# Performance work log

Hardware: AMD Instinct MI355X
Metric: run time of the kernel (lower is better)

## Reference

```python
import jax, jax.numpy as jnp
import numpy as np

N, T, S, E, H, DFF = 4, 2048, 2048, 512, 8, 2048
DH = E // H
EPS = 1e-5


def layer_norm(x, w, b):
    m = jnp.mean(x, axis=-1, keepdims=True)
    v = jnp.mean(jnp.square(x - m), axis=-1, keepdims=True)
    return (x - m) * jax.lax.rsqrt(v + EPS) * w + b


def mha(q, k, v, wq, bq, wk, bk, wv, bv, wo, bo, mask=None):
    # q: (N,Tq,E), k/v: (N,Tk,E); torch Linear convention: y = x @ W.T + b
    Nq, Tq, _ = q.shape
    Tk = k.shape[1]
    Q = (q @ wq.T + bq).reshape(Nq, Tq, H, DH).transpose(0, 2, 1, 3)  # (N,H,Tq,DH)
    K = (k @ wk.T + bk).reshape(Nq, Tk, H, DH).transpose(0, 2, 1, 3)
    V = (v @ wv.T + bv).reshape(Nq, Tk, H, DH).transpose(0, 2, 1, 3)
    scores = jnp.einsum('bhtd,bhsd->bhts', Q, K) * (1.0 / np.sqrt(DH))  # (N,H,Tq,Tk)
    if mask is not None:
        scores = jnp.where(mask, scores, jnp.float32(-1e9))
    attn = jax.nn.softmax(scores, axis=-1)
    out = jnp.einsum('bhts,bhsd->bhtd', attn, V)  # (N,H,Tq,DH)
    out = out.transpose(0, 2, 1, 3).reshape(Nq, Tq, E)
    return out @ wo.T + bo


def setup_inputs() -> dict:
    key = jax.random.key(0)
    ks = jax.random.split(key, 20)
    s = 0.02

    def lin(k, out_d, in_d):
        return jax.random.normal(k, (out_d, in_d), jnp.float32) * s

    inp = {
        'tgt': jax.random.normal(ks[0], (N, T, E), jnp.float32),
        'memory': jax.random.normal(ks[1], (N, S, E), jnp.float32),
        'tgt_mask': jnp.tril(jnp.ones((T, T), dtype=bool)),  # causal (T,T)
        # self-attention params
        'sa_wq': lin(ks[2], E, E), 'sa_bq': jnp.zeros((E,), jnp.float32),
        'sa_wk': lin(ks[3], E, E), 'sa_bk': jnp.zeros((E,), jnp.float32),
        'sa_wv': lin(ks[4], E, E), 'sa_bv': jnp.zeros((E,), jnp.float32),
        'sa_wo': lin(ks[5], E, E), 'sa_bo': jnp.zeros((E,), jnp.float32),
        # cross-attention params
        'ca_wq': lin(ks[6], E, E), 'ca_bq': jnp.zeros((E,), jnp.float32),
        'ca_wk': lin(ks[7], E, E), 'ca_bk': jnp.zeros((E,), jnp.float32),
        'ca_wv': lin(ks[8], E, E), 'ca_bv': jnp.zeros((E,), jnp.float32),
        'ca_wo': lin(ks[9], E, E), 'ca_bo': jnp.zeros((E,), jnp.float32),
        # FFN params
        'w1': lin(ks[10], DFF, E), 'b1': jnp.zeros((DFF,), jnp.float32),
        'w2': lin(ks[11], E, DFF), 'b2': jnp.zeros((E,), jnp.float32),
        # LayerNorm params
        'ln1_w': jnp.ones((E,), jnp.float32), 'ln1_b': jnp.zeros((E,), jnp.float32),
        'ln2_w': jnp.ones((E,), jnp.float32), 'ln2_b': jnp.zeros((E,), jnp.float32),
        'ln3_w': jnp.ones((E,), jnp.float32), 'ln3_b': jnp.zeros((E,), jnp.float32),
    }
    return inp


def reference(tgt, memory, tgt_mask,
              sa_wq, sa_bq, sa_wk, sa_bk, sa_wv, sa_bv, sa_wo, sa_bo,
              ca_wq, ca_bq, ca_wk, ca_bk, ca_wv, ca_bv, ca_wo, ca_bo,
              w1, b1, w2, b2,
              ln1_w, ln1_b, ln2_w, ln2_b, ln3_w, ln3_b):
    # stage 1: masked self-attention + residual + LN (dropout=0 / eval mode)
    sa = mha(tgt, tgt, tgt, sa_wq, sa_bq, sa_wk, sa_bk, sa_wv, sa_bv, sa_wo, sa_bo, mask=tgt_mask)
    x = layer_norm(tgt + sa, ln1_w, ln1_b)
    # stage 2: cross-attention over encoder memory + residual + LN
    ca = mha(x, memory, memory, ca_wq, ca_bq, ca_wk, ca_bk, ca_wv, ca_bv, ca_wo, ca_bo)
    x = layer_norm(x + ca, ln2_w, ln2_b)
    # stage 3: FFN (ReLU) + residual + LN
    mlp = jax.nn.relu(x @ w1.T + b1) @ w2.T + b2
    out = layer_norm(x + mlp, ln3_w, ln3_b)
    return out
```

## Files before the change

kernel.cpp:

```cpp
#include <hip/hip_runtime.h>
#include <hip/hip_bf16.h>
#include <cstdint>

typedef short short8 __attribute__((ext_vector_type(8)));
typedef short short4v __attribute__((ext_vector_type(4)));
typedef float f32x4 __attribute__((ext_vector_type(4)));
typedef float f32x16 __attribute__((ext_vector_type(16)));

#define GLL16(gp, lp) __builtin_amdgcn_global_load_lds( \
    (const __attribute__((address_space(1))) unsigned int*)(gp), \
    (__attribute__((address_space(3))) unsigned int*)(lp), 16, 0, 0)
#define WAITV(n) asm volatile("s_waitcnt vmcnt(" #n ")" ::: "memory")

__device__ __forceinline__ float bf2f(ushort u) {
    union { unsigned int i; float f; } v; v.i = ((unsigned int)u) << 16; return v.f;
}
__device__ __forceinline__ ushort f2bf(float f) {
    union { float f; unsigned int u; } v; v.f = f;
    unsigned int r = v.u + 0x7FFFu + ((v.u >> 16) & 1u);
    return (ushort)(r >> 16);
}
__device__ __forceinline__ int cvtpk_bf16(float lo, float hi) {
    int r;
    asm("v_cvt_pk_bf16_f32 %0, %1, %2" : "=v"(r) : "v"(lo), "v"(hi));
    return r;
}
__device__ __forceinline__ void plane32_swap(int& a, int& b) {
    asm volatile("v_permlane32_swap_b32 %0, %1" : "+v"(a), "+v"(b));
}
__device__ __forceinline__ float fast_exp2(float x) {
    float r;
    asm("v_exp_f32 %0, %1" : "=v"(r) : "v"(x));
    return r;
}

#define SCQ 0.18033688f

struct CvtArgs {
    const float* src[12];
    ushort*      dst[12];
};
__global__ __launch_bounds__(256) void f2b_all(CvtArgs a)
{
    int id = blockIdx.x;
    int seg, boff;
    if (id < 4096)       { seg = 0; boff = id; }
    else if (id < 8192)  { seg = 1; boff = id - 4096; }
    else if (id < 10240) { int t = id - 8192; seg = 2 + (t >> 8); boff = t & 255; }
    else if (id < 11264) { seg = 10; boff = id - 10240; }
    else                 { seg = 11; boff = id - 11264; }
    int i = (boff * 256 + threadIdx.x) * 4;
    f32x4 v = *(const f32x4*)(a.src[seg] + i);
    short4v o;
#pragma unroll
    for (int e = 0; e < 4; ++e) o[e] = (short)f2bf(v[e]);
    *(short4v*)(a.dst[seg] + i) = o;
}

template<int MODE, int DEPTH, int TN>
__global__ __launch_bounds__(256) void gemm_bt(
    const ushort* __restrict__ A, const ushort* __restrict__ W,
    const float* __restrict__ b0, const float* __restrict__ b1,
    const float* __restrict__ b2,
    ushort* __restrict__ C0, ushort* __restrict__ C1, ushort* __restrict__ C2,
    int M, int N, int K)
{
    constexpr int NI = TN / 32;
    constexpr int L  = (TN == 128) ? 4 : 3;
    __shared__ ushort As[DEPTH][128 * 32];
    __shared__ ushort Bs[DEPTH][TN * 32];
    const int tid = threadIdx.x;
    const int l  = tid & 63;
    const int w  = tid >> 6;
    const int wr = w >> 1, wc = w & 1;
    const int bn = blockIdx.x, bm = blockIdx.y;
    const int lg = l >> 4, li = l & 15;

    const ushort* Ab = A + (size_t)(bm * 128) * K;
    const ushort* Bb = W + (size_t)(bn * TN) * K;

    f32x4 acc[4][NI] = {};

    const int r0 = tid >> 2,         s0 = (tid & 3) ^ ((r0 >> 2) & 3);
    const int r1 = (tid + 256) >> 2, s1 = (tid & 3) ^ ((r1 >> 2) & 3);

    auto stage = [&](int buf, int kt) {
        const ushort* Ak = Ab + kt * 32;
        const ushort* Bk = Bb + kt * 32;
        GLL16(Ak + (size_t)r0 * K + s0 * 8, &As[buf][tid * 8]);
        GLL16(Ak + (size_t)r1 * K + s1 * 8, &As[buf][(tid + 256) * 8]);
        GLL16(Bk + (size_t)r0 * K + s0 * 8, &Bs[buf][tid * 8]);
        if (TN == 128)
            GLL16(Bk + (size_t)r1 * K + s1 * 8, &Bs[buf][(tid + 256) * 8]);
    };

    const int nk = K >> 5;
#pragma unroll
    for (int p = 0; p < DEPTH - 1; ++p)
        if (p < nk) stage(p, p);

    for (int kt = 0; kt < nk; ++kt) {
        const int b = kt & (DEPTH - 1);
        const int nxt = kt + DEPTH - 1;
        if (nxt < nk) stage(nxt & (DEPTH - 1), nxt);
        const int rem = nk - 1 - kt;
        const int fl = rem < DEPTH - 1 ? rem : DEPTH - 1;
        if (L == 4) {
            if (fl >= 3)      WAITV(12);
            else if (fl == 2) WAITV(8);
            else if (fl == 1) WAITV(4);
            else              WAITV(0);
        } else {
            if (fl >= 3)      WAITV(9);
            else if (fl == 2) WAITV(6);
            else if (fl == 1) WAITV(3);
            else              WAITV(0);
        }
        __builtin_amdgcn_s_barrier();
        __builtin_amdgcn_sched_barrier(0);

        short8 af[4], bfr[NI];
#pragma unroll
        for (int mi = 0; mi < 4; ++mi) {
            int row = wr * 64 + mi * 16 + li;
            int ch  = lg ^ ((row >> 2) & 3);
            af[mi] = *(const short8*)(&As[b][row * 32 + ch * 8]);
        }
#pragma unroll
        for (int ni = 0; ni < NI; ++ni) {
            int row = wc * (TN / 2) + ni * 16 + li;
            int ch  = lg ^ ((row >> 2) & 3);
            bfr[ni] = *(const short8*)(&Bs[b][row * 32 + ch * 8]);
        }
#pragma unroll
        for (int mi = 0; mi < 4; ++mi)
#pragma unroll
            for (int ni = 0; ni < NI; ++ni)
                acc[mi][ni] = __builtin_amdgcn_mfma_f32_16x16x32_bf16(
                    af[mi], bfr[ni], acc[mi][ni], 0, 0, 0);

        __builtin_amdgcn_sched_barrier(0);
        asm volatile("s_waitcnt lgkmcnt(0)" ::: "memory");
        __builtin_amdgcn_s_barrier();
    }

    const int crow0 = bm * 128 + wr * 64 + lg * 4;
    const int ccol0 = bn * TN + wc * (TN / 2) + li;
    const int sec = (MODE == 2 || MODE == 3) ? (bn >> 2) : 0;
    const float* bp = b0;
    ushort* Cw = C0;
    bool vsec = false;
    if (MODE == 2) {
        bp = (sec == 0) ? b0 : (sec == 1) ? b1 : b2;
        Cw = (sec == 0) ? C0 : (sec == 1) ? C1 : C2;
        vsec = (sec == 2);
    } else if (MODE == 3) {
        bp = (sec == 0) ? b0 : b1;
        Cw = (sec == 0) ? C0 : C1;
        vsec = (sec == 1);
    }
    const int Nout = (MODE == 2 || MODE == 3) ? 512 : N;
    const float scl = (MODE == 4 || (MODE == 2 && sec == 0)) ? SCQ : 1.f;

#pragma unroll
    for (int ni = 0; ni < NI; ++ni) {
        int col = ccol0 + ni * 16;
        int cl  = (MODE == 2 || MODE == 3) ? (col & 511) : col;
        float bv = bp[cl];
#pragma unroll
        for (int mi = 0; mi < 4; ++mi) {
            int row = crow0 + mi * 16;
            if (vsec) {
                int n = row >> 11, t = row & 2047;
                int h = cl >> 6,  d = cl & 63;
                size_t base = ((size_t)((n * 8 + h) * 64 + d)) * 2048 + t;
                short4v pk;
#pragma unroll
                for (int r = 0; r < 4; ++r) pk[r] = (short)f2bf(acc[mi][ni][r] + bv);
                *(short4v*)(Cw + base) = pk;
            } else {
#pragma unroll
                for (int r = 0; r < 4; ++r) {
                    float v = (acc[mi][ni][r] + bv) * scl;
                    if (MODE == 1) v = fmaxf(v, 0.f);
                    Cw[(size_t)(row + r) * Nout + cl] = f2bf(v);
                }
            }
        }
    }
}

template<bool CAUSAL>
__global__ __launch_bounds__(256) void attn_kernel(
    const ushort* __restrict__ Q, const ushort* __restrict__ K,
    const ushort* __restrict__ Vt, ushort* __restrict__ P0,
    ushort* __restrict__ P1, float* __restrict__ Ls, int Tk)
{
    __shared__ ushort SH[24576];
    const int tid = threadIdx.x;
    const int l = tid & 63, wq = tid >> 6;
    const int c = l & 31, hi = l >> 5;

    int qt, nh, ck;
    if (CAUSAL) {
        int g = (int)blockIdx.x >> 6;
        qt = (g < 8) ? (15 - g) : (g - 8);
        int r = blockIdx.x & 63;
        nh = r >> 1; ck = r & 1;
    } else {
        int pos = ((int)blockIdx.x & 7) * 128 + ((int)blockIdx.x >> 3);
        nh = pos >> 5; ck = (pos >> 4) & 1; qt = pos & 15;
    }
    const int q0 = qt * 128;
    const int n = nh >> 3, h = nh & 7;
    const int qw = q0 + wq * 32;
    const int qrow = qw + c;

    short8 qf[4];
#pragma unroll
    for (int s = 0; s < 4; ++s)
        qf[s] = *(const short8*)(Q + (size_t)(n * 2048 + qrow) * 512
                                   + h * 64 + s * 16 + hi * 8);

    f32x16 oacc[2] = {};
    f32x16 oS = {};
    const short ONE = (short)0x3F80;
    const short8 ones = {ONE, ONE, ONE, ONE, ONE, ONE, ONE, ONE};

    const ushort* Kbase = K + (size_t)(n * 2048) * 512 + h * 64;
    const ushort* Vbase = Vt + (size_t)nh * 64 * Tk;

    const int rowA = tid >> 3;
    const int cs0 = (((tid & 7) - (rowA >> 3)) & 7) ^ (rowA & 7);
    const int cs1 = (((tid & 7) - (rowA >> 3) + 4) & 7) ^ (rowA & 7);

    auto stage = [&](int buf, int j0) {
        ushort* kd = SH + buf * 4096;
        ushort* vd = SH + 12288 + buf * 4096;
        GLL16(Kbase + (size_t)(j0 + rowA) * 512 + cs0 * 8,      kd + tid * 8);
        GLL16(Kbase + (size_t)(j0 + rowA + 32) * 512 + cs1 * 8, kd + (tid + 256) * 8);
        GLL16(Vbase + (size_t)rowA * Tk + j0 + cs0 * 8,         vd + tid * 8);
        GLL16(Vbase + (size_t)(rowA + 32) * Tk + j0 + cs1 * 8,  vd + (tid + 256) * 8);
    };

    const int total = CAUSAL ? (2 * qt + 2) : (Tk >> 6);
    const int start = (ck * total) >> 1;
    const int cnt   = (((ck + 1) * total) >> 1) - start;

    if (cnt > 0) stage(0, start << 6);
    if (cnt > 1) stage(1, (start + 1) << 6);

    for (int s = 0; s < cnt; ++s) {
        const int b  = s % 3;
        const int j0 = (start + s) << 6;
        if (s + 1 < cnt) {
            WAITV(4);
        } else {
            WAITV(0);
        }
        __builtin_amdgcn_s_barrier();
        __builtin_amdgcn_sched_barrier(0);
        if (s + 2 < cnt) stage((s + 2) % 3, (start + s + 2) << 6);

        const bool active = !CAUSAL || (j0 < qw + 32);
        if (active) {
            const ushort* kls = SH + b * 4096;
            const ushort* vls = SH + 12288 + b * 4096;
            const bool domask = CAUSAL && (j0 + 64 > qw);

            f32x16 sacc[2] = {};
            __builtin_amdgcn_s_setprio(1);
#pragma unroll
            for (int ks = 0; ks < 4; ++ks) {
#pragma unroll
                for (int t2 = 0; t2 < 2; ++t2) {
                    int row = t2 * 32 + c;
                    int ch  = (((ks * 2 + hi) ^ (row & 7)) + (row >> 3)) & 7;
                    short8 kf = *(const short8*)(kls + row * 64 + ch * 8);
                    sacc[t2] = __builtin_amdgcn_mfma_f32_32x32x16_bf16(
                        kf, qf[ks], sacc[t2], 0, 0, 0);
                }
            }
            __builtin_amdgcn_s_setprio(0);

#pragma unroll
            for (int t2 = 0; t2 < 2; ++t2) {
                float pv[16];
#pragma unroll
                for (int reg = 0; reg < 16; ++reg) {
                    float p = fast_exp2(sacc[t2][reg]);
                    if (domask) {
                        int jg = j0 + t2 * 32 + (reg & 3) + 8 * (reg >> 2) + 4 * hi;
                        if (jg > qrow) p = 0.f;
                    }
                    pv[reg] = p;
                }
                int X0 = cvtpk_bf16(pv[0],  pv[1]),  Y0 = cvtpk_bf16(pv[2],  pv[3]);
                int X1 = cvtpk_bf16(pv[4],  pv[5]),  Y1 = cvtpk_bf16(pv[6],  pv[7]);
                int X2 = cvtpk_bf16(pv[8],  pv[9]),  Y2 = cvtpk_bf16(pv[10], pv[11]);
                int X3 = cvtpk_bf16(pv[12], pv[13]), Y3 = cvtpk_bf16(pv[14], pv[15]);
                plane32_swap(X0, X1); plane32_swap(Y0, Y1);
                plane32_swap(X2, X3); plane32_swap(Y2, Y3);
                union { int i[4]; short8 s; } pa0 = {{X0, Y0, X1, Y1}},
                                              pa1 = {{X2, Y2, X3, Y3}};
                __builtin_amdgcn_s_setprio(1);
                oS = __builtin_amdgcn_mfma_f32_32x32x16_bf16(pa0.s, ones, oS, 0, 0, 0);
                oS = __builtin_amdgcn_mfma_f32_32x32x16_bf16(pa1.s, ones, oS, 0, 0, 0);
#pragma unroll
                for (int sp = 0; sp < 2; ++sp) {
                    short8 pa = sp ? pa1.s : pa0.s;
#pragma unroll
                    for (int dc = 0; dc < 2; ++dc) {
                        int row = dc * 32 + c;
                        int ch  = (((t2 * 4 + sp * 2 + hi) ^ (row & 7)) + (row >> 3)) & 7;
                        short8 vb = *(const short8*)(vls + row * 64 + ch * 8);
                        oacc[dc] = __builtin_amdgcn_mfma_f32_32x32x16_bf16(
                            pa, vb, oacc[dc], 0, 0, 0);
                    }
                }
                __builtin_amdgcn_s_setprio(0);
            }
        }

        __builtin_amdgcn_sched_barrier(0);
        asm volatile("s_waitcnt lgkmcnt(0)" ::: "memory");
    }
    WAITV(0);

    ushort* Pw = ck ? P1 : P0;
    if (c == 0) {
#pragma unroll
        for (int reg = 0; reg < 16; ++reg) {
            int qloc = (reg & 3) + 8 * (reg >> 2) + 4 * hi;
            Ls[ck * 65536 + nh * 2048 + qw + qloc] = oS[reg];
        }
    }
#pragma unroll
    for (int dc = 0; dc < 2; ++dc)
#pragma unroll
        for (int reg = 0; reg < 16; ++reg) {
            int qloc = (reg & 3) + 8 * (reg >> 2) + 4 * hi;
            size_t off = (size_t)(n * 2048 + qw + qloc) * 512
                       + h * 64 + dc * 32 + c;
            Pw[off] = f2bf(oacc[dc][reg]);
        }
}

__global__ __launch_bounds__(256) void attn_merge(
    const ushort* __restrict__ P0, const ushort* __restrict__ P1,
    const float* __restrict__ Ls, ushort* __restrict__ out)
{
    const int row = blockIdx.x * 4 + (threadIdx.x >> 6);
    const int l = threadIdx.x & 63;
    const size_t off = (size_t)row * 512 + l * 8;
    const int n = row >> 11, q = row & 2047, h = l >> 3;
    const int lidx = (n * 8 + h) * 2048 + q;
    float linv = 1.f / (Ls[lidx] + Ls[65536 + lidx]);
    short8 a = *(const short8*)(P0 + off);
    short8 b = *(const short8*)(P1 + off);
    short8 o;
#pragma unroll
    for (int e = 0; e < 8; ++e)
        o[e] = (short)f2bf((bf2f((ushort)a[e]) + bf2f((ushort)b[e])) * linv);
    *(short8*)(out + off) = o;
}

template<int F32OUT>
__global__ __launch_bounds__(256) void ln_kernel(
    const ushort* __restrict__ X, const ushort* __restrict__ Y,
    const float* __restrict__ W, const float* __restrict__ B,
    void* __restrict__ outp)
{
    const int row = blockIdx.x * 4 + (threadIdx.x >> 6);
    const int l = threadIdx.x & 63;
    const size_t off = (size_t)row * 512 + l * 8;
    short8 xv = *(const short8*)(X + off);
    short8 yv = *(const short8*)(Y + off);
    float v[8], s = 0.f, s2 = 0.f;
#pragma unroll
    for (int e = 0; e < 8; ++e) {
        float f = bf2f((ushort)xv[e]) + bf2f((ushort)yv[e]);
        v[e] = f; s += f; s2 += f * f;
    }
#pragma unroll
    for (int m = 1; m < 64; m <<= 1) {
        s  += __shfl_xor(s,  m);
        s2 += __shfl_xor(s2, m);
    }
    float mean = s * (1.f / 512.f);
    float var  = s2 * (1.f / 512.f) - mean * mean;
    float rs   = rsqrtf(var + 1e-5f);
    f32x4 w0 = *(const f32x4*)(W + l * 8);
    f32x4 w1 = *(const f32x4*)(W + l * 8 + 4);
    f32x4 b0 = *(const f32x4*)(B + l * 8);
    f32x4 b1 = *(const f32x4*)(B + l * 8 + 4);
    float wv[8] = {w0[0], w0[1], w0[2], w0[3], w1[0], w1[1], w1[2], w1[3]};
    float bv[8] = {b0[0], b0[1], b0[2], b0[3], b1[0], b1[1], b1[2], b1[3]};
    if (F32OUT) {
        float* out = (float*)outp;
#pragma unroll
        for (int e = 0; e < 8; ++e)
            out[off + e] = (v[e] - mean) * rs * wv[e] + bv[e];
    } else {
        ushort* out = (ushort*)outp;
        short8 ov;
#pragma unroll
        for (int e = 0; e < 8; ++e)
            ov[e] = (short)f2bf((v[e] - mean) * rs * wv[e] + bv[e]);
        *(short8*)(out + off) = ov;
    }
}

extern "C" void kernel_launch(void* const* d_in, const int* in_sizes, int n_in,
                              void* d_out, int out_size, void* d_ws, size_t ws_size,
                              hipStream_t stream)
{
    (void)in_sizes; (void)n_in; (void)out_size; (void)ws_size;
    const float* tgt  = (const float*)d_in[0];
    const float* mem  = (const float*)d_in[1];
    const float* sa_wq = (const float*)d_in[3];
    const float* sa_bq = (const float*)d_in[4];
    const float* sa_wk = (const float*)d_in[5];
    const float* sa_bk = (const float*)d_in[6];
    const float* sa_wv = (const float*)d_in[7];
    const float* sa_bv = (const float*)d_in[8];
    const float* sa_wo = (const float*)d_in[9];
    const float* sa_bo = (const float*)d_in[10];
    const float* ca_wq = (const float*)d_in[11];
    const float* ca_bq = (const float*)d_in[12];
    const float* ca_wk = (const float*)d_in[13];
    const float* ca_bk = (const float*)d_in[14];
    const float* ca_wv = (const float*)d_in[15];
    const float* ca_bv = (const float*)d_in[16];
    const float* ca_wo = (const float*)d_in[17];
    const float* ca_bo = (const float*)d_in[18];
    const float* w1    = (const float*)d_in[19];
    const float* b1    = (const float*)d_in[20];
    const float* w2    = (const float*)d_in[21];
    const float* b2    = (const float*)d_in[22];
    const float* ln1w  = (const float*)d_in[23];
    const float* ln1b  = (const float*)d_in[24];
    const float* ln2w  = (const float*)d_in[25];
    const float* ln2b  = (const float*)d_in[26];
    const float* ln3w  = (const float*)d_in[27];
    const float* ln3b  = (const float*)d_in[28];

    const size_t SE = (size_t)8192 * 512;
    const size_t EE = (size_t)512 * 512;
    ushort* ws = (ushort*)d_ws;
    ushort* Wb   = ws;
    ushort* bsqkv = Wb;
    ushort* bswo  = Wb + 3 * EE;
    ushort* bcwq  = Wb + 4 * EE;
    ushort* bckv  = Wb + 5 * EE;
    ushort* bcwo  = Wb + 7 * EE;
    ushort* bw1   = Wb + 8 * EE;
    ushort* bw2   = bw1 + 4 * EE;
    ushort* tgtb = Wb + 16 * EE;
    ushort* memb = tgtb + SE;
    ushort* Qb   = memb + SE;
    ushort* Kb   = Qb + SE;
    ushort* Vb   = Kb + SE;
    ushort* X1   = Vb + SE;
    ushort* AO   = X1 + SE;
    float*  LsBuf = (float*)(AO + SE);
    ushort* PO   = Qb;
    ushort* X2   = tgtb;
    ushort* Hb   = Qb;

    dim3 blk(256);
    dim3 gqkv(12, 64);
    dim3 gkv(8, 64);
    dim3 g64n(8, 64);
    dim3 g2048(16, 64);
    dim3 ga(1024);
    dim3 gln(2048);

    CvtArgs ca;
    ca.src[0] = tgt;    ca.dst[0] = tgtb;
    ca.src[1] = mem;    ca.dst[1] = memb;
    ca.src[2] = sa_wq;  ca.dst[2] = bsqkv;
    ca.src[3] = sa_wk;  ca.dst[3] = bsqkv + EE;
    ca.src[4] = sa_wv;  ca.dst[4] = bsqkv + 2 * EE;
    ca.src[5] = sa_wo;  ca.dst[5] = bswo;
    ca.src[6] = ca_wq;  ca.dst[6] = bcwq;
    ca.src[7] = ca_wk;  ca.dst[7] = bckv;
    ca.src[8] = ca_wv;  ca.dst[8] = bckv + EE;
    ca.src[9] = ca_wo;  ca.dst[9] = bcwo;
    ca.src[10] = w1;    ca.dst[10] = bw1;
    ca.src[11] = w2;    ca.dst[11] = bw2;
    f2b_all<<<12288, blk, 0, stream>>>(ca);

    gemm_bt<2, 2, 128><<<gqkv, blk, 0, stream>>>(tgtb, bsqkv, sa_bq, sa_bk, sa_bv,
                                                 Qb, Kb, Vb, 8192, 1536, 512);
    attn_kernel<true><<<ga, blk, 0, stream>>>(Qb, Kb, Vb, AO, X1, LsBuf, 2048);
    attn_merge<<<gln, blk, 0, stream>>>(AO, X1, LsBuf, AO);
    gemm_bt<0, 4, 64><<<g64n, blk, 0, stream>>>(AO, bswo, sa_bo, nullptr, nullptr,
                                                PO, nullptr, nullptr, 8192, 512, 512);
    ln_kernel<0><<<gln, blk, 0, stream>>>(tgtb, PO, ln1w, ln1b, X1);

    gemm_bt<4, 4, 64><<<g64n, blk, 0, stream>>>(X1, bcwq, ca_bq, nullptr, nullptr,
                                                Qb, nullptr, nullptr, 8192, 512, 512);
    gemm_bt<3, 2, 128><<<gkv, blk, 0, stream>>>(memb, bckv, ca_bk, ca_bv, nullptr,
                                                Kb, Vb, nullptr, 8192, 1024, 512);
    attn_kernel<false><<<ga, blk, 0, stream>>>(Qb, Kb, Vb, AO, tgtb, LsBuf, 2048);
    attn_merge<<<gln, blk, 0, stream>>>(AO, tgtb, LsBuf, AO);
    gemm_bt<0, 4, 64><<<g64n, blk, 0, stream>>>(AO, bcwo, ca_bo, nullptr, nullptr,
                                                PO, nullptr, nullptr, 8192, 512, 512);
    ln_kernel<0><<<gln, blk, 0, stream>>>(X1, PO, ln2w, ln2b, X2);

    gemm_bt<1, 2, 128><<<g2048, blk, 0, stream>>>(X2, bw1, b1, nullptr, nullptr,
                                                  Hb, nullptr, nullptr, 8192, 2048, 512);
    gemm_bt<0, 4, 64><<<g64n, blk, 0, stream>>>(Hb, bw2, b2, nullptr, nullptr,
                                                AO, nullptr, nullptr, 8192, 512, 2048);
    ln_kernel<1><<<gln, blk, 0, stream>>>(X2, AO, ln3w, ln3b, d_out);
}
```

Before: 295.6 us.

## Split-K the N=512 output GEMMs and sum partials inside LayerNorm

```diff
diff --git a/kernel.cpp b/kernel.cpp
--- a/kernel.cpp
+++ b/kernel.cpp
@@ -74,10 +74,12 @@
     const int w  = tid >> 6;
     const int wr = w >> 1, wc = w & 1;
     const int bn = blockIdx.x, bm = blockIdx.y;
+    const int kz = (MODE == 5) ? blockIdx.z : 0;
+    const int Keff = (MODE == 5) ? (K >> 1) : K;
     const int lg = l >> 4, li = l & 15;
 
-    const ushort* Ab = A + (size_t)(bm * 128) * K;
-    const ushort* Bb = W + (size_t)(bn * TN) * K;
+    const ushort* Ab = A + (size_t)(bm * 128) * K + (size_t)kz * Keff;
+    const ushort* Bb = W + (size_t)(bn * TN) * K + (size_t)kz * Keff;
 
     f32x4 acc[4][NI] = {};
 
@@ -94,7 +96,7 @@
             GLL16(Bk + (size_t)r1 * K + s1 * 8, &Bs[buf][(tid + 256) * 8]);
     };
 
-    const int nk = K >> 5;
+    const int nk = Keff >> 5;
 #pragma unroll
     for (int p = 0; p < DEPTH - 1; ++p)
         if (p < nk) stage(p, p);
@@ -158,6 +160,8 @@
         bp = (sec == 0) ? b0 : b1;
         Cw = (sec == 0) ? C0 : C1;
         vsec = (sec == 1);
+    } else if (MODE == 5) {
+        Cw = kz ? C1 : C0;
     }
     const int Nout = (MODE == 2 || MODE == 3) ? 512 : N;
     const float scl = (MODE == 4 || (MODE == 2 && sec == 0)) ? SCQ : 1.f;
@@ -166,7 +170,7 @@
     for (int ni = 0; ni < NI; ++ni) {
         int col = ccol0 + ni * 16;
         int cl  = (MODE == 2 || MODE == 3) ? (col & 511) : col;
-        float bv = bp[cl];
+        float bv = (MODE == 5 && kz) ? 0.f : bp[cl];
 #pragma unroll
         for (int mi = 0; mi < 4; ++mi) {
             int row = crow0 + mi * 16;
@@ -365,9 +369,10 @@
     *(short8*)(out + off) = o;
 }
 
-template<int F32OUT>
+template<int F32OUT, int NY>
 __global__ __launch_bounds__(256) void ln_kernel(
     const ushort* __restrict__ X, const ushort* __restrict__ Y,
+    const ushort* __restrict__ Y2,
     const float* __restrict__ W, const float* __restrict__ B,
     void* __restrict__ outp)
 {
@@ -376,10 +381,13 @@
     const size_t off = (size_t)row * 512 + l * 8;
     short8 xv = *(const short8*)(X + off);
     short8 yv = *(const short8*)(Y + off);
+    short8 y2v = {};
+    if (NY == 2) y2v = *(const short8*)(Y2 + off);
     float v[8], s = 0.f, s2 = 0.f;
 #pragma unroll
     for (int e = 0; e < 8; ++e) {
         float f = bf2f((ushort)xv[e]) + bf2f((ushort)yv[e]);
+        if (NY == 2) f += bf2f((ushort)y2v[e]);
         v[e] = f; s += f; s2 += f * f;
     }
 #pragma unroll
@@ -464,7 +472,6 @@
     ushort* X1   = Vb + SE;
     ushort* AO   = X1 + SE;
     float*  LsBuf = (float*)(AO + SE);
-    ushort* PO   = Qb;
     ushort* X2   = tgtb;
     ushort* Hb   = Qb;
 
@@ -472,6 +479,7 @@
     dim3 gqkv(12, 64);
     dim3 gkv(8, 64);
     dim3 g64n(8, 64);
+    dim3 g64k2(8, 64, 2);
     dim3 g2048(16, 64);
     dim3 ga(1024);
     dim3 gln(2048);
@@ -495,9 +503,9 @@
                                                  Qb, Kb, Vb, 8192, 1536, 512);
     attn_kernel<true><<<ga, blk, 0, stream>>>(Qb, Kb, Vb, AO, X1, LsBuf, 2048);
     attn_merge<<<gln, blk, 0, stream>>>(AO, X1, LsBuf, AO);
-    gemm_bt<0, 4, 64><<<g64n, blk, 0, stream>>>(AO, bswo, sa_bo, nullptr, nullptr,
-                                                PO, nullptr, nullptr, 8192, 512, 512);
-    ln_kernel<0><<<gln, blk, 0, stream>>>(tgtb, PO, ln1w, ln1b, X1);
+    gemm_bt<5, 4, 64><<<g64k2, blk, 0, stream>>>(AO, bswo, sa_bo, nullptr, nullptr,
+                                                 Qb, Kb, nullptr, 8192, 512, 512);
+    ln_kernel<0, 2><<<gln, blk, 0, stream>>>(tgtb, Qb, Kb, ln1w, ln1b, X1);
 
     gemm_bt<4, 4, 64><<<g64n, blk, 0, stream>>>(X1, bcwq, ca_bq, nullptr, nullptr,
                                                 Qb, nullptr, nullptr, 8192, 512, 512);
@@ -505,13 +513,13 @@
                                                 Kb, Vb, nullptr, 8192, 1024, 512);
     attn_kernel<false><<<ga, blk, 0, stream>>>(Qb, Kb, Vb, AO, tgtb, LsBuf, 2048);
     attn_merge<<<gln, blk, 0, stream>>>(AO, tgtb, LsBuf, AO);
-    gemm_bt<0, 4, 64><<<g64n, blk, 0, stream>>>(AO, bcwo, ca_bo, nullptr, nullptr,
-                                                PO, nullptr, nullptr, 8192, 512, 512);
-    ln_kernel<0><<<gln, blk, 0, stream>>>(X1, PO, ln2w, ln2b, X2);
+    gemm_bt<5, 4, 64><<<g64k2, blk, 0, stream>>>(AO, bcwo, ca_bo, nullptr, nullptr,
+                                                 Qb, Kb, nullptr, 8192, 512, 512);
+    ln_kernel<0, 2><<<gln, blk, 0, stream>>>(X1, Qb, Kb, ln2w, ln2b, X2);
 
     gemm_bt<1, 2, 128><<<g2048, blk, 0, stream>>>(X2, bw1, b1, nullptr, nullptr,
                                                   Hb, nullptr, nullptr, 8192, 2048, 512);
-    gemm_bt<0, 4, 64><<<g64n, blk, 0, stream>>>(Hb, bw2, b2, nullptr, nullptr,
-                                                AO, nullptr, nullptr, 8192, 512, 2048);
-    ln_kernel<1><<<gln, blk, 0, stream>>>(X2, AO, ln3w, ln3b, d_out);
-}
+    gemm_bt<5, 4, 64><<<g64k2, blk, 0, stream>>>(Hb, bw2, b2, nullptr, nullptr,
+                                                 AO, memb, nullptr, 8192, 512, 2048);
+    ln_kernel<1, 2><<<gln, blk, 0, stream>>>(X2, AO, memb, ln3w, ln3b, d_out);
+}
```

Result: slower. 311.6 us (+5.4%).
